# Performance work log

Measured on AMD Instinct MI355X. Metric: run time of the kernel, lower is better.

## Reference

```python
import jax, jax.numpy as jnp
import numpy as np
import math

D = 1280      # embed_dim ('650M')
H = 20        # n_head
DH = D // H   # d_hidden = 64
DFF = 4 * D   # r_ff = 4
LN_EPS = 1e-5


def layer_norm(x, gamma, beta):
    mu = jnp.mean(x, axis=-1, keepdims=True)
    var = jnp.var(x, axis=-1, keepdims=True)
    return (x - mu) * jax.lax.rsqrt(var + LN_EPS) * gamma + beta


def setup_inputs() -> dict:
    key = jax.random.key(0)
    ks = jax.random.split(key, 16)
    B, L = 2, 2048
    x = jax.random.normal(ks[0], (B, L, D), dtype=jnp.float32)
    y = jax.random.normal(ks[1], (B, L, D), dtype=jnp.float32)  # dm_embeds (unused by module)
    s_qkv = 1.0 / math.sqrt(D)
    Wq = jax.random.uniform(ks[2], (D, D), jnp.float32, -s_qkv, s_qkv)
    Wk = jax.random.uniform(ks[3], (D, D), jnp.float32, -s_qkv, s_qkv)
    Wv = jax.random.uniform(ks[4], (D, D), jnp.float32, -s_qkv, s_qkv)
    Wo = jax.random.uniform(ks[5], (D, D), jnp.float32, -s_qkv, s_qkv)
    bo = jnp.zeros((D,), jnp.float32)
    W1 = jax.random.normal(ks[6], (D, DFF), jnp.float32) * math.sqrt(2.0 / D)  # kaiming
    b1 = jnp.zeros((DFF,), jnp.float32)
    W2 = jax.random.uniform(ks[7], (DFF, D), jnp.float32, -1.0 / math.sqrt(DFF), 1.0 / math.sqrt(DFF))
    b2 = jnp.zeros((D,), jnp.float32)
    g1 = jnp.ones((D,), jnp.float32); be1 = jnp.zeros((D,), jnp.float32)
    g2 = jnp.ones((D,), jnp.float32); be2 = jnp.zeros((D,), jnp.float32)
    return dict(x=x, y=y, Wq=Wq, Wk=Wk, Wv=Wv, Wo=Wo, bo=bo,
                W1=W1, b1=b1, W2=W2, b2=b2, g1=g1, be1=be1, g2=g2, be2=be2)


def reference(x, y, Wq, Wk, Wv, Wo, bo, W1, b1, W2, b2, g1, be1, g2, be2):
    B, L, _ = x.shape
    scaling = 1.0 / math.sqrt(DH)
    # --- pre-norm self-attention ---
    xn = layer_norm(x, g1, be1)
    q = (xn @ Wq).reshape(B, L, H, DH) * scaling
    k = (xn @ Wk).reshape(B, L, H, DH)
    v = (xn @ Wv).reshape(B, L, H, DH)
    scores = jnp.einsum('bqhd,bkhd->bhqk', q, k)
    attn = jax.nn.softmax(scores, axis=-1)
    o = jnp.einsum('bhqk,bkhd->bqhd', attn, v).reshape(B, L, D)
    x = x + (o @ Wo + bo)
    # --- pre-norm FFN ---
    xn = layer_norm(x, g2, be2)
    h = jax.nn.relu(xn @ W1 + b1)
    x = x + (h @ W2 + b2)
    return x
```

## Files before the change

kernel.cpp:

```cpp
#include <hip/hip_runtime.h>

typedef short bf16x8 __attribute__((ext_vector_type(8)));
typedef short bf16x4 __attribute__((ext_vector_type(4)));
typedef float f32x4 __attribute__((ext_vector_type(4)));
typedef unsigned short u16;

#define GL16(g, l) __builtin_amdgcn_global_load_lds( \
    (const __attribute__((address_space(1))) void*)(g), \
    (__attribute__((address_space(3))) void*)(l), 16, 0, 0)

__device__ __forceinline__ u16 f2bf(float f) {
  union { float f; unsigned u; } v; v.f = f;
  return (u16)((v.u + 0x7fffu + ((v.u >> 16) & 1u)) >> 16);
}

__global__ __launch_bounds__(256) void ln_kernel(
    const float* __restrict__ x, const float* __restrict__ g,
    const float* __restrict__ b, u16* __restrict__ out) {
  const int row = blockIdx.x, tid = threadIdx.x;
  const float4* xr = (const float4*)(x + (size_t)row * 1280);
  float4 v1 = xr[tid];
  float4 v2 = make_float4(0.f, 0.f, 0.f, 0.f);
  if (tid < 64) v2 = xr[256 + tid];
  float s = v1.x + v1.y + v1.z + v1.w + v2.x + v2.y + v2.z + v2.w;
  float q = v1.x * v1.x + v1.y * v1.y + v1.z * v1.z + v1.w * v1.w +
            v2.x * v2.x + v2.y * v2.y + v2.z * v2.z + v2.w * v2.w;
#pragma unroll
  for (int off = 32; off >= 1; off >>= 1) {
    s += __shfl_xor(s, off);
    q += __shfl_xor(q, off);
  }
  __shared__ float sm[8];
  if ((tid & 63) == 0) { sm[tid >> 6] = s; sm[4 + (tid >> 6)] = q; }
  __syncthreads();
  s = sm[0] + sm[1] + sm[2] + sm[3];
  q = sm[4] + sm[5] + sm[6] + sm[7];
  const float mean = s * (1.0f / 1280.0f);
  const float rstd = rsqrtf(q * (1.0f / 1280.0f) - mean * mean + 1e-5f);
  const float4* gr = (const float4*)g;
  const float4* br = (const float4*)b;
  u16* orow = out + (size_t)row * 1280;
  {
    float4 gg = gr[tid], bb = br[tid];
    ushort4 o;
    o.x = f2bf((v1.x - mean) * rstd * gg.x + bb.x);
    o.y = f2bf((v1.y - mean) * rstd * gg.y + bb.y);
    o.z = f2bf((v1.z - mean) * rstd * gg.z + bb.z);
    o.w = f2bf((v1.w - mean) * rstd * gg.w + bb.w);
    *(ushort4*)&orow[tid * 4] = o;
  }
  if (tid < 64) {
    float4 gg = gr[256 + tid], bb = br[256 + tid];
    ushort4 o;
    o.x = f2bf((v2.x - mean) * rstd * gg.x + bb.x);
    o.y = f2bf((v2.y - mean) * rstd * gg.y + bb.y);
    o.z = f2bf((v2.z - mean) * rstd * gg.z + bb.z);
    o.w = f2bf((v2.w - mean) * rstd * gg.w + bb.w);
    *(ushort4*)&orow[(256 + tid) * 4] = o;
  }
}

__global__ __launch_bounds__(256) void tconv_kernel(
    const float* __restrict__ src, u16* __restrict__ dst,
    int rows, int cols, float scale) {
  __shared__ float t[64][33];
  const int tid = threadIdx.x;
  const size_t c0 = (size_t)blockIdx.x * 64, r0 = (size_t)blockIdx.y * 32;
  const int ty = tid >> 4, col4 = tid & 15;
#pragma unroll
  for (int i = 0; i < 2; ++i) {
    const int row = ty + i * 16;
    float4 v = *(const float4*)&src[(r0 + row) * cols + c0 + col4 * 4];
    t[col4 * 4 + 0][row] = v.x;
    t[col4 * 4 + 1][row] = v.y;
    t[col4 * 4 + 2][row] = v.z;
    t[col4 * 4 + 3][row] = v.w;
  }
  __syncthreads();
  const int c = tid >> 2, rb = (tid & 3) * 8;
  ushort4 o1, o2;
  o1.x = f2bf(t[c][rb + 0] * scale); o1.y = f2bf(t[c][rb + 1] * scale);
  o1.z = f2bf(t[c][rb + 2] * scale); o1.w = f2bf(t[c][rb + 3] * scale);
  o2.x = f2bf(t[c][rb + 4] * scale); o2.y = f2bf(t[c][rb + 5] * scale);
  o2.z = f2bf(t[c][rb + 6] * scale); o2.w = f2bf(t[c][rb + 7] * scale);
  u16* d = &dst[(c0 + c) * rows + r0 + rb];
  *(ushort4*)d = o1;
  *(ushort4*)(d + 4) = o2;
}

__global__ __launch_bounds__(256) void vtrans_kernel(const u16* __restrict__ qkv,
                                                     u16* __restrict__ vt) {
  __shared__ u16 t[64][65];
  const int tx = threadIdx.x & 63, ty = threadIdx.x >> 6;
  const int t0 = blockIdx.x * 64, bh = blockIdx.y, b = bh / 20, h = bh % 20;
  const u16* src = qkv + (size_t)b * 2048 * 3840 + 2560 + h * 64;
  for (int i = ty; i < 64; i += 4) t[i][tx] = src[(size_t)(t0 + i) * 3840 + tx];
  __syncthreads();
  u16* dst = vt + (size_t)bh * 64 * 2048 + t0;
  for (int i = ty; i < 64; i += 4) dst[(size_t)i * 2048 + tx] = t[tx][i];
}

__global__ __launch_bounds__(256) void initadd_kernel(
    const float* __restrict__ src, const float* __restrict__ bias,
    float* __restrict__ out) {
  const size_t i = (size_t)blockIdx.x * 256 + threadIdx.x;
  float4 v = ((const float4*)src)[i];
  float4 b = ((const float4*)bias)[i % 320];
  v.x += b.x; v.y += b.y; v.z += b.z; v.w += b.w;
  ((float4*)out)[i] = v;
}

template <int EPI>
__device__ __forceinline__ void gemm_body(
    const u16* __restrict__ A, const u16* __restrict__ BT,
    const float* __restrict__ bias, void* __restrict__ out,
    int M, int N, int K, int kSteps) {
  __shared__ __attribute__((aligned(16))) u16 Als[3][128 * 32];
  __shared__ __attribute__((aligned(16))) u16 Bls[3][128 * 32];
  const int tid = threadIdx.x;
  const int w = tid >> 6, lane = tid & 63;
  const int lo = lane & 15, hi = lane >> 4;
  const int wm = w >> 1, wn = w & 1;
  const int gx = gridDim.x, gxy = gx * gridDim.y;
  const int nwg = gxy * gridDim.z;
  int s = blockIdx.x + gx * blockIdx.y + gxy * blockIdx.z;
  s = (s & 7) * (nwg >> 3) + (s >> 3);
  const int bz = s / gxy; s -= bz * gxy;
  const int by = s / gx;  const int bx = s - by * gx;
  const size_t m0 = (size_t)by * 128, n0 = (size_t)bx * 128;
  const int kt0 = bz * kSteps;
  f32x4 acc[4][4] = {};
  const int srow = w * 32 + (lane >> 2);
  const int scol = ((lane & 3) ^ ((lane >> 3) & 3)) * 8;
  const int rsw = (lo >> 1) & 3;
#define STAGE(buf, kt)                                                        \
  do {                                                                        \
    const size_t kb = (size_t)(kt) * 32 + scol;                               \
    GL16(&A[(m0 + srow) * K + kb],       &Als[buf][(w * 2 + 0) * 512]);       \
    GL16(&A[(m0 + srow + 16) * K + kb],  &Als[buf][(w * 2 + 1) * 512]);       \
    GL16(&BT[(n0 + srow) * K + kb],      &Bls[buf][(w * 2 + 0) * 512]);       \
    GL16(&BT[(n0 + srow + 16) * K + kb], &Bls[buf][(w * 2 + 1) * 512]);       \
  } while (0)
  STAGE(0, kt0 + 0);
  STAGE(1, kt0 + 1);
  int cur = 0;
  for (int t = 0; t < kSteps; ++t) {
    if (t + 1 < kSteps) asm volatile("s_waitcnt vmcnt(4)" ::: "memory");
    else                asm volatile("s_waitcnt vmcnt(0)" ::: "memory");
    __builtin_amdgcn_s_barrier();
    __builtin_amdgcn_sched_barrier(0);
    const int nxt = (cur == 0) ? 2 : cur - 1;
    if (t + 2 < kSteps) STAGE(nxt, kt0 + t + 2);
    bf16x8 af[4], bfr[4];
#pragma unroll
    for (int mi = 0; mi < 4; ++mi)
      af[mi] = *(const bf16x8*)&Als[cur][(wm * 64 + mi * 16 + lo) * 32 + ((hi ^ rsw) * 8)];
#pragma unroll
    for (int ni = 0; ni < 4; ++ni)
      bfr[ni] = *(const bf16x8*)&Bls[cur][(wn * 64 + ni * 16 + lo) * 32 + ((hi ^ rsw) * 8)];
#pragma unroll
    for (int mi = 0; mi < 4; ++mi)
#pragma unroll
      for (int ni = 0; ni < 4; ++ni)
        acc[mi][ni] = __builtin_amdgcn_mfma_f32_16x16x32_bf16(
            af[mi], bfr[ni], acc[mi][ni], 0, 0, 0);
    cur = (cur == 2) ? 0 : cur + 1;
  }
#undef STAGE
#pragma unroll
  for (int ni = 0; ni < 4; ++ni) {
    const size_t col = n0 + wn * 64 + ni * 16 + lo;
    const float bv = (EPI == 1) ? bias[col] : 0.0f;
#pragma unroll
    for (int mi = 0; mi < 4; ++mi) {
      const size_t rb = m0 + wm * 64 + mi * 16 + hi * 4;
#pragma unroll
      for (int r = 0; r < 4; ++r) {
        const size_t idx = (rb + r) * N + col;
        float v = acc[mi][ni][r];
        if (EPI == 0) {
          ((u16*)out)[idx] = f2bf(v);
        } else if (EPI == 1) {
          v += bv;
          v = fmaxf(v, 0.0f);
          ((u16*)out)[idx] = f2bf(v);
        } else {
          atomicAdd(&((float*)out)[idx], v);
        }
      }
    }
  }
}

__global__ __launch_bounds__(256, 3) void gemm_qkv(
    const u16* __restrict__ A, const u16* __restrict__ BT,
    void* __restrict__ out, int M, int N, int K, int kSteps) {
  gemm_body<0>(A, BT, nullptr, out, M, N, K, kSteps);
}
__global__ __launch_bounds__(256, 3) void gemm_oproj(
    const u16* __restrict__ A, const u16* __restrict__ BT,
    void* __restrict__ out, int M, int N, int K, int kSteps) {
  gemm_body<3>(A, BT, nullptr, out, M, N, K, kSteps);
}
__global__ __launch_bounds__(256, 3) void gemm_ffn1(
    const u16* __restrict__ A, const u16* __restrict__ BT,
    const float* __restrict__ bias, void* __restrict__ out,
    int M, int N, int K, int kSteps) {
  gemm_body<1>(A, BT, bias, out, M, N, K, kSteps);
}
__global__ __launch_bounds__(256, 3) void gemm_ffn2(
    const u16* __restrict__ A, const u16* __restrict__ BT,
    void* __restrict__ out, int M, int N, int K, int kSteps) {
  gemm_body<3>(A, BT, nullptr, out, M, N, K, kSteps);
}

__global__ __launch_bounds__(256) void attn_kernel(
    const u16* __restrict__ qkv, const u16* __restrict__ vt,
    u16* __restrict__ aout) {
  __shared__ __attribute__((aligned(16))) u16 Klds[64 * 64];
  __shared__ __attribute__((aligned(16))) u16 Vlds[64 * 64];
  __shared__ __attribute__((aligned(16))) u16 Plds[4][16][72];
  const int tid = threadIdx.x;
  const int w = tid >> 6, lane = tid & 63;
  const int lo = lane & 15, hi = lane >> 4;
  const int qt = blockIdx.x, bh = blockIdx.y;
  const int b = bh / 20, h = bh % 20;
  const size_t qrow = (size_t)b * 2048 + qt * 64 + w * 16 + lo;
  bf16x8 qf[2];
  qf[0] = *(const bf16x8*)&qkv[qrow * 3840 + h * 64 + hi * 8];
  qf[1] = *(const bf16x8*)&qkv[qrow * 3840 + h * 64 + 32 + hi * 8];
  float m_i = -1e30f, l_i = 0.0f;
  f32x4 accO[4] = {};
  const int srow = lane >> 3;
  const int scol = ((lane & 7) ^ srow) * 8;
  const u16* kbase = qkv + (size_t)b * 2048 * 3840 + 1280 + h * 64;
  const u16* vbase = vt + (size_t)bh * 64 * 2048;
  for (int kt = 0; kt < 32; ++kt) {
#pragma unroll
    for (int c = 0; c < 2; ++c) {
      const int chunk = w * 2 + c;
      const int row = chunk * 8 + srow;
      GL16(kbase + (size_t)(kt * 64 + row) * 3840 + scol, &Klds[chunk * 512]);
      GL16(vbase + (size_t)row * 2048 + kt * 64 + scol, &Vlds[chunk * 512]);
    }
    __syncthreads();
    f32x4 s4[4] = {};
#pragma unroll
    for (int st = 0; st < 4; ++st) {
      const int row = st * 16 + lo;
      const int sw = (row & 7) << 3;
#pragma unroll
      for (int ks = 0; ks < 2; ++ks) {
        bf16x8 a = *(const bf16x8*)&Klds[row * 64 + ((ks * 32 + hi * 8) ^ sw)];
        s4[st] = __builtin_amdgcn_mfma_f32_16x16x32_bf16(a, qf[ks], s4[st], 0, 0, 0);
      }
    }
    float tm = -1e30f;
#pragma unroll
    for (int st = 0; st < 4; ++st)
#pragma unroll
      for (int r = 0; r < 4; ++r) tm = fmaxf(tm, s4[st][r]);
    tm = fmaxf(tm, __shfl_xor(tm, 16));
    tm = fmaxf(tm, __shfl_xor(tm, 32));
    const float mnew = fmaxf(m_i, tm);
    const float corr = __expf(m_i - mnew);
    float ps = 0.0f;
#pragma unroll
    for (int st = 0; st < 4; ++st)
#pragma unroll
      for (int r = 0; r < 4; ++r) {
        const float p = __expf(s4[st][r] - mnew);
        s4[st][r] = p;
        ps += p;
      }
    ps += __shfl_xor(ps, 16);
    ps += __shfl_xor(ps, 32);
    l_i = l_i * corr + ps;
    m_i = mnew;
#pragma unroll
    for (int st = 0; st < 4; ++st) {
      bf16x4 pk;
      pk[0] = (short)f2bf(s4[st][0]);
      pk[1] = (short)f2bf(s4[st][1]);
      pk[2] = (short)f2bf(s4[st][2]);
      pk[3] = (short)f2bf(s4[st][3]);
      *(bf16x4*)&Plds[w][lo][st * 16 + hi * 4] = pk;
    }
    float cr[4];
#pragma unroll
    for (int r = 0; r < 4; ++r) cr[r] = __shfl(corr, hi * 4 + r);
#pragma unroll
    for (int d = 0; d < 4; ++d)
#pragma unroll
      for (int r = 0; r < 4; ++r) accO[d][r] *= cr[r];
    asm volatile("s_waitcnt lgkmcnt(0)" ::: "memory");
    __builtin_amdgcn_sched_barrier(0);
#pragma unroll
    for (int ks = 0; ks < 2; ++ks) {
      bf16x8 pa = *(const bf16x8*)&Plds[w][lo][ks * 32 + hi * 8];
#pragma unroll
      for (int d = 0; d < 4; ++d) {
        const int row = d * 16 + lo;
        bf16x8 vb = *(const bf16x8*)
            &Vlds[row * 64 + ((ks * 32 + hi * 8) ^ ((row & 7) << 3))];
        accO[d] = __builtin_amdgcn_mfma_f32_16x16x32_bf16(pa, vb, accO[d], 0, 0, 0);
      }
    }
    __syncthreads();
  }
  float linv[4];
#pragma unroll
  for (int r = 0; r < 4; ++r) linv[r] = 1.0f / __shfl(l_i, hi * 4 + r);
  const size_t orow0 = (size_t)b * 2048 + qt * 64 + w * 16 + hi * 4;
#pragma unroll
  for (int d = 0; d < 4; ++d)
#pragma unroll
    for (int r = 0; r < 4; ++r)
      aout[(orow0 + r) * 1280 + h * 64 + d * 16 + lo] =
          f2bf(accO[d][r] * linv[r]);
}

extern "C" void kernel_launch(void* const* d_in, const int* in_sizes, int n_in,
                              void* d_out, int out_size, void* d_ws, size_t ws_size,
                              hipStream_t stream) {
  const float* x   = (const float*)d_in[0];
  const float* Wq  = (const float*)d_in[2];
  const float* Wk  = (const float*)d_in[3];
  const float* Wv  = (const float*)d_in[4];
  const float* Wo  = (const float*)d_in[5];
  const float* bo  = (const float*)d_in[6];
  const float* W1  = (const float*)d_in[7];
  const float* b1  = (const float*)d_in[8];
  const float* W2  = (const float*)d_in[9];
  const float* b2  = (const float*)d_in[10];
  const float* g1  = (const float*)d_in[11];
  const float* be1 = (const float*)d_in[12];
  const float* g2  = (const float*)d_in[13];
  const float* be2 = (const float*)d_in[14];

  u16* xn   = (u16*)d_ws;
  u16* Wqkv = xn + (size_t)4096 * 1280;
  u16* WoT  = Wqkv + (size_t)3840 * 1280;
  u16* W1T  = WoT + (size_t)1280 * 1280;
  u16* W2T  = W1T + (size_t)5120 * 1280;
  u16* aOut = W2T + (size_t)1280 * 5120;
  float* x1 = (float*)(aOut + (size_t)4096 * 1280);
  u16* qkvb = (u16*)(x1 + (size_t)4096 * 1280);
  u16* vtb  = qkvb + (size_t)4096 * 3840;
  u16* hbuf = qkvb;

  ln_kernel<<<4096, 256, 0, stream>>>(x, g1, be1, xn);
  tconv_kernel<<<dim3(20, 40), 256, 0, stream>>>(Wq, Wqkv, 1280, 1280, 0.125f);
  tconv_kernel<<<dim3(20, 40), 256, 0, stream>>>(Wk, Wqkv + (size_t)1280 * 1280, 1280, 1280, 1.0f);
  tconv_kernel<<<dim3(20, 40), 256, 0, stream>>>(Wv, Wqkv + (size_t)2 * 1280 * 1280, 1280, 1280, 1.0f);
  tconv_kernel<<<dim3(20, 40), 256, 0, stream>>>(Wo, WoT, 1280, 1280, 1.0f);
  tconv_kernel<<<dim3(80, 40), 256, 0, stream>>>(W1, W1T, 1280, 5120, 1.0f);
  tconv_kernel<<<dim3(20, 160), 256, 0, stream>>>(W2, W2T, 5120, 1280, 1.0f);
  gemm_qkv<<<dim3(30, 32, 1), 256, 0, stream>>>(xn, Wqkv, qkvb, 4096, 3840, 1280, 40);
  vtrans_kernel<<<dim3(32, 40), 256, 0, stream>>>(qkvb, vtb);
  attn_kernel<<<dim3(32, 40), 256, 0, stream>>>(qkvb, vtb, aOut);
  initadd_kernel<<<5120, 256, 0, stream>>>(x, bo, x1);
  gemm_oproj<<<dim3(10, 32, 2), 256, 0, stream>>>(aOut, WoT, x1, 4096, 1280, 1280, 20);
  ln_kernel<<<4096, 256, 0, stream>>>(x1, g2, be2, xn);
  gemm_ffn1<<<dim3(40, 32, 1), 256, 0, stream>>>(xn, W1T, b1, hbuf, 4096, 5120, 1280, 40);
  initadd_kernel<<<5120, 256, 0, stream>>>(x1, b2, (float*)d_out);
  gemm_ffn2<<<dim3(10, 32, 2), 256, 0, stream>>>(hbuf, W2T, d_out, 4096, 1280, 5120, 80);
  (void)in_sizes; (void)n_in; (void)out_size; (void)ws_size;
}
```

Baseline: 437.8 us.

## Triple-buffer attention K/V loads and use exp2 softmax with lazy rescaling

The attention kernel gets a three-stage ring of K/V LDS buffers filled by async global-to-LDS loads two tiles ahead, and waits with vmcnt plus a single barrier per iteration in place of two syncthreads. Softmax switches to exp2 with log2(e) folded into the Q weight scale, and skips the output rescale when the running max grows by at most 8. P is packed to bf16 with a hardware pack instruction, and the grid is reordered so head/batch varies fastest. These changes aim to overlap memory latency with MFMA work and trim VALU work, at the cost of more LDS (which may lower occupancy) and somewhat wider exponent headroom in the accumulators.

```diff
diff --git a/kernel.cpp b/kernel.cpp
--- a/kernel.cpp
+++ b/kernel.cpp
@@ -12,6 +12,20 @@
 __device__ __forceinline__ u16 f2bf(float f) {
   union { float f; unsigned u; } v; v.f = f;
   return (u16)((v.u + 0x7fffu + ((v.u >> 16) & 1u)) >> 16);
+}
+
+__device__ __forceinline__ float exp2_(float x) {
+#if __has_builtin(__builtin_amdgcn_exp2f)
+  return __builtin_amdgcn_exp2f(x);
+#else
+  return __expf(x * 0.69314718056f);
+#endif
+}
+
+__device__ __forceinline__ unsigned cvtpk(float a, float b) {
+  unsigned r;
+  asm("v_cvt_pk_bf16_f32 %0, %1, %2" : "=v"(r) : "v"(a), "v"(b));
+  return r;
 }
 
 __global__ __launch_bounds__(256) void ln_kernel(
@@ -217,13 +231,13 @@
 __global__ __launch_bounds__(256) void attn_kernel(
     const u16* __restrict__ qkv, const u16* __restrict__ vt,
     u16* __restrict__ aout) {
-  __shared__ __attribute__((aligned(16))) u16 Klds[64 * 64];
-  __shared__ __attribute__((aligned(16))) u16 Vlds[64 * 64];
+  __shared__ __attribute__((aligned(16))) u16 Kls[3][64 * 64];
+  __shared__ __attribute__((aligned(16))) u16 Vls[3][64 * 64];
   __shared__ __attribute__((aligned(16))) u16 Plds[4][16][72];
   const int tid = threadIdx.x;
   const int w = tid >> 6, lane = tid & 63;
   const int lo = lane & 15, hi = lane >> 4;
-  const int qt = blockIdx.x, bh = blockIdx.y;
+  const int bh = blockIdx.x, qt = blockIdx.y;
   const int b = bh / 20, h = bh % 20;
   const size_t qrow = (size_t)b * 2048 + qt * 64 + w * 16 + lo;
   bf16x8 qf[2];
@@ -235,15 +249,28 @@
   const int scol = ((lane & 7) ^ srow) * 8;
   const u16* kbase = qkv + (size_t)b * 2048 * 3840 + 1280 + h * 64;
   const u16* vbase = vt + (size_t)bh * 64 * 2048;
+#define ASTAGE(buf, kt)                                                       \
+  do {                                                                        \
+    _Pragma("unroll")                                                         \
+    for (int c = 0; c < 2; ++c) {                                             \
+      const int chunk = w * 2 + c;                                            \
+      const int row = chunk * 8 + srow;                                       \
+      GL16(kbase + (size_t)((kt) * 64 + row) * 3840 + scol,                   \
+           &Kls[buf][chunk * 512]);                                           \
+      GL16(vbase + (size_t)row * 2048 + (kt) * 64 + scol,                     \
+           &Vls[buf][chunk * 512]);                                           \
+    }                                                                         \
+  } while (0)
+  ASTAGE(0, 0);
+  ASTAGE(1, 1);
+  int cur = 0;
   for (int kt = 0; kt < 32; ++kt) {
-#pragma unroll
-    for (int c = 0; c < 2; ++c) {
-      const int chunk = w * 2 + c;
-      const int row = chunk * 8 + srow;
-      GL16(kbase + (size_t)(kt * 64 + row) * 3840 + scol, &Klds[chunk * 512]);
-      GL16(vbase + (size_t)row * 2048 + kt * 64 + scol, &Vlds[chunk * 512]);
-    }
-    __syncthreads();
+    if (kt + 1 < 32) asm volatile("s_waitcnt vmcnt(4)" ::: "memory");
+    else             asm volatile("s_waitcnt vmcnt(0)" ::: "memory");
+    __builtin_amdgcn_s_barrier();
+    __builtin_amdgcn_sched_barrier(0);
+    const int nxt = (cur == 0) ? 2 : cur - 1;
+    if (kt + 2 < 32) ASTAGE(nxt, kt + 2);
     f32x4 s4[4] = {};
 #pragma unroll
     for (int st = 0; st < 4; ++st) {
@@ -251,48 +278,48 @@
       const int sw = (row & 7) << 3;
 #pragma unroll
       for (int ks = 0; ks < 2; ++ks) {
-        bf16x8 a = *(const bf16x8*)&Klds[row * 64 + ((ks * 32 + hi * 8) ^ sw)];
+        bf16x8 a = *(const bf16x8*)&Kls[cur][row * 64 + ((ks * 32 + hi * 8) ^ sw)];
         s4[st] = __builtin_amdgcn_mfma_f32_16x16x32_bf16(a, qf[ks], s4[st], 0, 0, 0);
       }
     }
-    float tm = -1e30f;
-#pragma unroll
-    for (int st = 0; st < 4; ++st)
-#pragma unroll
-      for (int r = 0; r < 4; ++r) tm = fmaxf(tm, s4[st][r]);
+    float tm = fmaxf(fmaxf(fmaxf(s4[0][0], s4[0][1]), fmaxf(s4[0][2], s4[0][3])),
+                     fmaxf(fmaxf(s4[1][0], s4[1][1]), fmaxf(s4[1][2], s4[1][3])));
+    tm = fmaxf(tm, fmaxf(fmaxf(fmaxf(s4[2][0], s4[2][1]), fmaxf(s4[2][2], s4[2][3])),
+                         fmaxf(fmaxf(s4[3][0], s4[3][1]), fmaxf(s4[3][2], s4[3][3]))));
     tm = fmaxf(tm, __shfl_xor(tm, 16));
     tm = fmaxf(tm, __shfl_xor(tm, 32));
-    const float mnew = fmaxf(m_i, tm);
-    const float corr = __expf(m_i - mnew);
+    if (!__all(tm <= m_i + 8.0f)) {
+      const float mnew = fmaxf(m_i, tm);
+      const float corr = exp2_(m_i - mnew);
+      m_i = mnew;
+      float cr[4];
+#pragma unroll
+      for (int r = 0; r < 4; ++r) cr[r] = __shfl(corr, hi * 4 + r);
+#pragma unroll
+      for (int d = 0; d < 4; ++d)
+#pragma unroll
+        for (int r = 0; r < 4; ++r) accO[d][r] *= cr[r];
+      l_i *= corr;
+    }
     float ps = 0.0f;
 #pragma unroll
     for (int st = 0; st < 4; ++st)
 #pragma unroll
       for (int r = 0; r < 4; ++r) {
-        const float p = __expf(s4[st][r] - mnew);
+        const float p = exp2_(s4[st][r] - m_i);
         s4[st][r] = p;
         ps += p;
       }
     ps += __shfl_xor(ps, 16);
     ps += __shfl_xor(ps, 32);
-    l_i = l_i * corr + ps;
-    m_i = mnew;
+    l_i += ps;
 #pragma unroll
     for (int st = 0; st < 4; ++st) {
-      bf16x4 pk;
-      pk[0] = (short)f2bf(s4[st][0]);
-      pk[1] = (short)f2bf(s4[st][1]);
-      pk[2] = (short)f2bf(s4[st][2]);
-      pk[3] = (short)f2bf(s4[st][3]);
-      *(bf16x4*)&Plds[w][lo][st * 16 + hi * 4] = pk;
-    }
-    float cr[4];
-#pragma unroll
-    for (int r = 0; r < 4; ++r) cr[r] = __shfl(corr, hi * 4 + r);
-#pragma unroll
-    for (int d = 0; d < 4; ++d)
-#pragma unroll
-      for (int r = 0; r < 4; ++r) accO[d][r] *= cr[r];
+      uint2 pk;
+      pk.x = cvtpk(s4[st][0], s4[st][1]);
+      pk.y = cvtpk(s4[st][2], s4[st][3]);
+      *(uint2*)&Plds[w][lo][st * 16 + hi * 4] = pk;
+    }
     asm volatile("s_waitcnt lgkmcnt(0)" ::: "memory");
     __builtin_amdgcn_sched_barrier(0);
 #pragma unroll
@@ -302,12 +329,13 @@
       for (int d = 0; d < 4; ++d) {
         const int row = d * 16 + lo;
         bf16x8 vb = *(const bf16x8*)
-            &Vlds[row * 64 + ((ks * 32 + hi * 8) ^ ((row & 7) << 3))];
+            &Vls[cur][row * 64 + ((ks * 32 + hi * 8) ^ ((row & 7) << 3))];
         accO[d] = __builtin_amdgcn_mfma_f32_16x16x32_bf16(pa, vb, accO[d], 0, 0, 0);
       }
     }
-    __syncthreads();
-  }
+    cur = (cur == 2) ? 0 : cur + 1;
+  }
+#undef ASTAGE
   float linv[4];
 #pragma unroll
   for (int r = 0; r < 4; ++r) linv[r] = 1.0f / __shfl(l_i, hi * 4 + r);
@@ -349,8 +377,9 @@
   u16* vtb  = qkvb + (size_t)4096 * 3840;
   u16* hbuf = qkvb;
 
+  const float qscale = 0.125f * 1.4426950408889634f;
   ln_kernel<<<4096, 256, 0, stream>>>(x, g1, be1, xn);
-  tconv_kernel<<<dim3(20, 40), 256, 0, stream>>>(Wq, Wqkv, 1280, 1280, 0.125f);
+  tconv_kernel<<<dim3(20, 40), 256, 0, stream>>>(Wq, Wqkv, 1280, 1280, qscale);
   tconv_kernel<<<dim3(20, 40), 256, 0, stream>>>(Wk, Wqkv + (size_t)1280 * 1280, 1280, 1280, 1.0f);
   tconv_kernel<<<dim3(20, 40), 256, 0, stream>>>(Wv, Wqkv + (size_t)2 * 1280 * 1280, 1280, 1280, 1.0f);
   tconv_kernel<<<dim3(20, 40), 256, 0, stream>>>(Wo, WoT, 1280, 1280, 1.0f);
@@ -358,7 +387,7 @@
   tconv_kernel<<<dim3(20, 160), 256, 0, stream>>>(W2, W2T, 5120, 1280, 1.0f);
   gemm_qkv<<<dim3(30, 32, 1), 256, 0, stream>>>(xn, Wqkv, qkvb, 4096, 3840, 1280, 40);
   vtrans_kernel<<<dim3(32, 40), 256, 0, stream>>>(qkvb, vtb);
-  attn_kernel<<<dim3(32, 40), 256, 0, stream>>>(qkvb, vtb, aOut);
+  attn_kernel<<<dim3(40, 32), 256, 0, stream>>>(qkvb, vtb, aOut);
   initadd_kernel<<<5120, 256, 0, stream>>>(x, bo, x1);
   gemm_oproj<<<dim3(10, 32, 2), 256, 0, stream>>>(aOut, WoT, x1, 4096, 1280, 1280, 20);
   ln_kernel<<<4096, 256, 0, stream>>>(x1, g2, be2, xn);
```

Result: slower. 463.7 us (+5.9%).
